# Kernel optimization log

Measured on AMD Instinct MI355X. Metric: run time of the kernel, lower is better.

## Reference

```python
import jax, jax.numpy as jnp
import numpy as np

B, T, C = 512, 256, 384
HEAD = 64

def setup_inputs() -> dict:
    key = jax.random.key(0)
    k1, k2, k3, k4 = jax.random.split(key, 4)
    x = jax.random.normal(k1, (B, T, C), dtype=jnp.float32)
    Wq = jax.random.normal(k2, (C, HEAD), dtype=jnp.float32) * (C ** -0.5)
    Wk = jax.random.normal(k3, (C, HEAD), dtype=jnp.float32) * (C ** -0.5)
    Wv = jax.random.normal(k4, (C, HEAD), dtype=jnp.float32) * (C ** -0.5)
    return {"x": x, "Wq": Wq, "Wk": Wk, "Wv": Wv}

def reference(x, Wq, Wk, Wv):
    # projections (Linear with bias=False): x @ W
    q = jnp.einsum('btc,ch->bth', x, Wq)   # [B,T,H]
    k = jnp.einsum('btc,ch->bth', x, Wk)   # [B,T,H]
    v = jnp.einsum('btc,ch->bth', x, Wv)   # [B,T,H]
    Cdim = x.shape[-1]
    # NOTE: original scales by C**-0.5 where C = nEmbd (not headSize)
    scores = jnp.einsum('bth,bsh->bts', q, k) * (Cdim ** -0.5)  # [B,T,T]
    Tlen = x.shape[1]
    causal = jnp.tril(jnp.ones((Tlen, Tlen), dtype=bool))
    scores = jnp.where(causal, scores, -jnp.inf)
    wei = jax.nn.softmax(scores, axis=-1)
    # dropout omitted (eval mode / deterministic reference)
    out = jnp.einsum('bts,bsh->bth', wei, v)  # [B,T,H]
    return out
```

## Files before the change

### kernel.cpp

```cpp
#include <hip/hip_runtime.h>

#define B_ 512
#define T_ 256
#define C_ 384
#define H_ 64
#define WT2_HALF  36864
#define WT2_TOTAL (2 * WT2_HALF)

typedef __bf16 bf16;
typedef bf16  bf16x8 __attribute__((ext_vector_type(8)));
typedef float f32x4  __attribute__((ext_vector_type(4)));

__global__ void prep_wt2(const float* __restrict__ Wq,
                         const float* __restrict__ Wk,
                         const float* __restrict__ Wv,
                         bf16* __restrict__ wt2)
{
    int idx = blockIdx.x * 256 + threadIdx.x;
    if (idx >= WT2_TOTAL) return;
    int half = idx / WT2_HALF;
    int rem  = idx % WT2_HALF;
    int s    = rem >> 3;
    int e    = rem & 7;
    int mc   = s / 24;
    int kkc  = (s % 24) ^ (mc & 7);
    int mat  = mc >> 6;
    int col  = mc & 63;
    int k    = half * 192 + kkc * 8 + e;
    const float* W = (mat == 0) ? Wq : (mat == 1) ? Wk : Wv;
    wt2[idx] = (bf16)W[k * H_ + col];
}

__device__ __forceinline__ bf16x8 cvt8(float4 a, float4 b)
{
    bf16x8 r;
    r[0] = (bf16)a.x; r[1] = (bf16)a.y; r[2] = (bf16)a.z; r[3] = (bf16)a.w;
    r[4] = (bf16)b.x; r[5] = (bf16)b.y; r[6] = (bf16)b.z; r[7] = (bf16)b.w;
    return r;
}

__device__ __forceinline__ void gload_lds16(const bf16* g, bf16* l)
{
    __builtin_amdgcn_global_load_lds(
        (const __attribute__((address_space(1))) void*)g,
        (__attribute__((address_space(3))) void*)l,
        16, 0, 0);
}

#define SWZ(row, col) ((col) ^ (((row) & 7) << 3))

__device__ __forceinline__ const bf16x8* wts_frag(const bf16* wt_s, int mc, int kk)
{
    int byte = ((mc * 192 + kk) * 2) ^ ((mc & 7) << 4);
    return reinterpret_cast<const bf16x8*>(reinterpret_cast<const char*>(wt_s) + byte);
}

template<int USE_WT>
__global__
__attribute__((amdgpu_flat_work_group_size(512, 512)))
__attribute__((amdgpu_waves_per_eu(2, 2)))
void head_fused7(const float* __restrict__ x,
                 const float* __restrict__ Wq,
                 const float* __restrict__ Wk,
                 const float* __restrict__ Wv,
                 const bf16* __restrict__ wt2,
                 float* __restrict__ out)
{
    __shared__ bf16 wt_s[3 * 64 * 192];
    __shared__ bf16 k_s[T_ * 64];
    __shared__ bf16 vT_s[H_ * 256];
    __shared__ bf16 p_s[8 * 16 * 64];

    const int tid  = threadIdx.x;
    const int wave = tid >> 6;
    const int lane = tid & 63;
    const int lr   = lane & 15;
    const int lg   = lane >> 4;

    const int b = blockIdx.x;
    const float* xb = x + (size_t)b * T_ * C_;
    bf16* pw = &p_s[wave * 16 * 64];

    const int mt0 = wave;
    const int mt1 = 15 - wave;

    bf16x8 qf[2][2];

    f32x4 acc[2][3][4];
    #pragma unroll
    for (int t = 0; t < 2; ++t)
        #pragma unroll
        for (int a = 0; a < 3; ++a)
            #pragma unroll
            for (int nw = 0; nw < 4; ++nw)
                acc[t][a][nw] = (f32x4){0.f, 0.f, 0.f, 0.f};

    #pragma unroll 1
    for (int half = 0; half < 2; ++half) {
        __syncthreads();
        if (USE_WT) {
            #pragma unroll
            for (int c = 0; c < 9; ++c) {
                const bf16* g = wt2 + half * WT2_HALF + (c * 512 + tid) * 8;
                bf16* l = wt_s + (c * 512 + wave * 64) * 8;
                gload_lds16(g, l);
            }
        } else {
            #pragma unroll
            for (int c = 0; c < 9; ++c) {
                int f16 = c * 512 + tid;
                int mc  = f16 / 24;
                int kkc = f16 % 24;
                int mat = mc >> 6, col = mc & 63;
                const float* W = (mat == 0) ? Wq : (mat == 1) ? Wk : Wv;
                bf16x8 vv;
                #pragma unroll
                for (int j = 0; j < 8; ++j)
                    vv[j] = (bf16)W[(half * 192 + kkc * 8 + j) * H_ + col];
                int byte = ((mc * 192 + kkc * 8) * 2) ^ ((mc & 7) << 4);
                *reinterpret_cast<bf16x8*>(reinterpret_cast<char*>(wt_s) + byte) = vv;
            }
        }

        bf16x8 af0[6], af1[6];
        {
            const float* xr = xb + (mt0 * 16 + lr) * C_ + half * 192 + lg * 8;
            float4 t0[6], t1[6];
            #pragma unroll
            for (int ks = 0; ks < 6; ++ks) {
                t0[ks] = *reinterpret_cast<const float4*>(xr + ks * 32);
                t1[ks] = *reinterpret_cast<const float4*>(xr + ks * 32 + 4);
            }
            #pragma unroll
            for (int ks = 0; ks < 6; ++ks) af0[ks] = cvt8(t0[ks], t1[ks]);
        }
        {
            const float* xr = xb + (mt1 * 16 + lr) * C_ + half * 192 + lg * 8;
            float4 t0[6], t1[6];
            #pragma unroll
            for (int ks = 0; ks < 6; ++ks) {
                t0[ks] = *reinterpret_cast<const float4*>(xr + ks * 32);
                t1[ks] = *reinterpret_cast<const float4*>(xr + ks * 32 + 4);
            }
            #pragma unroll
            for (int ks = 0; ks < 6; ++ks) af1[ks] = cvt8(t0[ks], t1[ks]);
        }
        __syncthreads();

        #pragma unroll
        for (int ks = 0; ks < 6; ++ks) {
            const int kk = ks * 32 + lg * 8;
            #pragma unroll
            for (int mat = 0; mat < 3; ++mat) {
                #pragma unroll
                for (int nw = 0; nw < 4; ++nw) {
                    bf16x8 bfr = *wts_frag(wt_s, mat * 64 + nw * 16 + lr, kk);
                    acc[0][mat][nw] = __builtin_amdgcn_mfma_f32_16x16x32_bf16(
                        af0[ks], bfr, acc[0][mat][nw], 0, 0, 0);
                    acc[1][mat][nw] = __builtin_amdgcn_mfma_f32_16x16x32_bf16(
                        af1[ks], bfr, acc[1][mat][nw], 0, 0, 0);
                }
            }
        }
    }

    #pragma unroll
    for (int tile = 0; tile < 2; ++tile) {
        const int mt = tile ? mt1 : mt0;
        #pragma unroll
        for (int nw = 0; nw < 4; ++nw) {
            #pragma unroll
            for (int r = 0; r < 4; ++r) {
                int row = mt * 16 + lg * 4 + r;
                int col = nw * 16 + lr;
                k_s[row * 64 + SWZ(row, col)]   = (bf16)acc[tile][1][nw][r];
                vT_s[col * 256 + SWZ(col, row)] = (bf16)acc[tile][2][nw][r];
            }
        }
        #pragma unroll
        for (int nw = 0; nw < 4; ++nw) {
            #pragma unroll
            for (int r = 0; r < 4; ++r) {
                int row = lg * 4 + r;
                pw[row * 64 + SWZ(row, nw * 16 + lr)] = (bf16)acc[tile][0][nw][r];
            }
        }
        asm volatile("s_waitcnt lgkmcnt(0)" ::: "memory");
        __builtin_amdgcn_sched_barrier(0);
        qf[tile][0] = *reinterpret_cast<const bf16x8*>(&pw[lr * 64 + SWZ(lr, lg * 8)]);
        qf[tile][1] = *reinterpret_cast<const bf16x8*>(&pw[lr * 64 + SWZ(lr, 32 + lg * 8)]);
    }
    __syncthreads();

    const float scale = 0.051031036307982884f;

    #pragma unroll
    for (int p = 0; p < 2; ++p) {
        const int mt  = p ? mt1 : mt0;
        const int nkt = mt + 1;

        float m[4], l[4];
        f32x4 oacc[4];
        #pragma unroll
        for (int r = 0; r < 4; ++r) { m[r] = -1e30f; l[r] = 0.f; }
        #pragma unroll
        for (int n = 0; n < 4; ++n) oacc[n] = (f32x4){0.f, 0.f, 0.f, 0.f};

        #pragma unroll
        for (int h = 0; h < 2; ++h) {
            const int vh = (nkt - h * 8) < 8 ? (nkt - h * 8) : 8;
            if (vh > 0) {
                float s[8][4];
                #pragma unroll
                for (int j = 0; j < 8; ++j) {
                    const int kt = h * 8 + j;
                    if (j < vh) {
                        bf16x8 kf0 = *reinterpret_cast<const bf16x8*>(
                            &k_s[(kt * 16 + lr) * 64 + SWZ(lr, lg * 8)]);
                        bf16x8 kf1 = *reinterpret_cast<const bf16x8*>(
                            &k_s[(kt * 16 + lr) * 64 + SWZ(lr, 32 + lg * 8)]);
                        f32x4 sc = (f32x4){0.f, 0.f, 0.f, 0.f};
                        sc = __builtin_amdgcn_mfma_f32_16x16x32_bf16(qf[p][0], kf0, sc, 0, 0, 0);
                        sc = __builtin_amdgcn_mfma_f32_16x16x32_bf16(qf[p][1], kf1, sc, 0, 0, 0);
                        #pragma unroll
                        for (int r = 0; r < 4; ++r) {
                            float v = sc[r] * scale;
                            if (kt == mt && lr > lg * 4 + r) v = -1e30f;
                            s[j][r] = v;
                        }
                    } else {
                        #pragma unroll
                        for (int r = 0; r < 4; ++r) s[j][r] = -1e30f;
                    }
                }

                float f[4];
                #pragma unroll
                for (int r = 0; r < 4; ++r) {
                    float pm = s[0][r];
                    #pragma unroll
                    for (int j = 1; j < 8; ++j) pm = fmaxf(pm, s[j][r]);
                    pm = fmaxf(pm, __shfl_xor(pm, 1));
                    pm = fmaxf(pm, __shfl_xor(pm, 2));
                    pm = fmaxf(pm, __shfl_xor(pm, 4));
                    pm = fmaxf(pm, __shfl_xor(pm, 8));
                    float nm = fmaxf(m[r], pm);
                    f[r] = __expf(m[r] - nm);
                    m[r] = nm;
                    l[r] *= f[r];
                }
                #pragma unroll
                for (int n = 0; n < 4; ++n)
                    #pragma unroll
                    for (int r = 0; r < 4; ++r)
                        oacc[n][r] *= f[r];

                #pragma unroll
                for (int r = 0; r < 4; ++r) {
                    float t = 0.f;
                    #pragma unroll
                    for (int j = 0; j < 8; ++j) {
                        float e = __expf(s[j][r] - m[r]);
                        s[j][r] = e;
                        t += e;
                    }
                    t += __shfl_xor(t, 1);
                    t += __shfl_xor(t, 2);
                    t += __shfl_xor(t, 4);
                    t += __shfl_xor(t, 8);
                    l[r] += t;
                }

                const int nkk = (vh + 1) >> 1;
                #pragma unroll
                for (int kkl = 0; kkl < 4; ++kkl) {
                    if (kkl < nkk) {
                        const int kk = h * 4 + kkl;
                        #pragma unroll
                        for (int r = 0; r < 4; ++r) {
                            int row = lg * 4 + r;
                            pw[row * 64 + SWZ(row, lr)]      = (bf16)s[2 * kkl][r];
                            pw[row * 64 + SWZ(row, 16 + lr)] = (bf16)s[2 * kkl + 1][r];
                        }
                        asm volatile("s_waitcnt lgkmcnt(0)" ::: "memory");
                        __builtin_amdgcn_sched_barrier(0);
                        bf16x8 pf = *reinterpret_cast<const bf16x8*>(
                            &pw[lr * 64 + SWZ(lr, lg * 8)]);
                        #pragma unroll
                        for (int n = 0; n < 4; ++n) {
                            bf16x8 vf = *reinterpret_cast<const bf16x8*>(
                                &vT_s[(n * 16 + lr) * 256 + SWZ(lr, kk * 32 + lg * 8)]);
                            oacc[n] = __builtin_amdgcn_mfma_f32_16x16x32_bf16(pf, vf, oacc[n], 0, 0, 0);
                        }
                    }
                }
            }
        }

        float rin[4];
        #pragma unroll
        for (int r = 0; r < 4; ++r) rin[r] = 1.0f / l[r];
        float* op = out + ((size_t)b * T_ + mt * 16) * H_;
        #pragma unroll
        for (int n = 0; n < 4; ++n)
            #pragma unroll
            for (int r = 0; r < 4; ++r)
                op[(lg * 4 + r) * H_ + n * 16 + lr] = oacc[n][r] * rin[r];
    }
}

extern "C" void kernel_launch(void* const* d_in, const int* in_sizes, int n_in,
                              void* d_out, int out_size, void* d_ws, size_t ws_size,
                              hipStream_t stream)
{
    (void)in_sizes; (void)n_in; (void)out_size;
    const float* x  = (const float*)d_in[0];
    const float* Wq = (const float*)d_in[1];
    const float* Wk = (const float*)d_in[2];
    const float* Wv = (const float*)d_in[3];
    float* o = (float*)d_out;

    if (ws_size >= (size_t)(WT2_TOTAL * sizeof(bf16))) {
        bf16* wt2 = (bf16*)d_ws;
        prep_wt2<<<dim3((WT2_TOTAL + 255) / 256), dim3(256), 0, stream>>>(Wq, Wk, Wv, wt2);
        head_fused7<1><<<dim3(B_), dim3(512), 0, stream>>>(x, Wq, Wk, Wv, wt2, o);
    } else {
        head_fused7<0><<<dim3(B_), dim3(512), 0, stream>>>(x, Wq, Wk, Wv, nullptr, o);
    }
}
```

Measured before the change: 78.12 us.

## Split fused attention into projection and attention kernels via bf16 workspace

```diff
diff --git a/kernel.cpp b/kernel.cpp
--- a/kernel.cpp
+++ b/kernel.cpp
@@ -4,12 +4,19 @@
 #define T_ 256
 #define C_ 384
 #define H_ 64
+
+typedef __bf16 bf16;
+typedef bf16  bf16x8 __attribute__((ext_vector_type(8)));
+typedef bf16  bf16x4 __attribute__((ext_vector_type(4)));
+typedef float f32x4  __attribute__((ext_vector_type(4)));
+
 #define WT2_HALF  36864
 #define WT2_TOTAL (2 * WT2_HALF)
-
-typedef __bf16 bf16;
-typedef bf16  bf16x8 __attribute__((ext_vector_type(8)));
-typedef float f32x4  __attribute__((ext_vector_type(4)));
+#define QKV_ELEMS (B_ * T_ * H_)
+#define Q_OFF  (1u << 20)
+#define K_OFF  (Q_OFF + (unsigned)QKV_ELEMS * 2u)
+#define V_OFF  (K_OFF + (unsigned)QKV_ELEMS * 2u)
+#define WS_NEED ((size_t)V_OFF + (size_t)QKV_ELEMS * 2u)
 
 __global__ void prep_wt2(const float* __restrict__ Wq,
                          const float* __restrict__ Wk,
@@ -56,20 +63,17 @@
 }
 
 template<int USE_WT>
-__global__
-__attribute__((amdgpu_flat_work_group_size(512, 512)))
-__attribute__((amdgpu_waves_per_eu(2, 2)))
-void head_fused7(const float* __restrict__ x,
+__global__ __launch_bounds__(512, 2)
+void proj_kernel(const float* __restrict__ x,
                  const float* __restrict__ Wq,
                  const float* __restrict__ Wk,
                  const float* __restrict__ Wv,
                  const bf16* __restrict__ wt2,
-                 float* __restrict__ out)
+                 bf16* __restrict__ q_ws,
+                 bf16* __restrict__ k_ws,
+                 bf16* __restrict__ vT_ws)
 {
     __shared__ bf16 wt_s[3 * 64 * 192];
-    __shared__ bf16 k_s[T_ * 64];
-    __shared__ bf16 vT_s[H_ * 256];
-    __shared__ bf16 p_s[8 * 16 * 64];
 
     const int tid  = threadIdx.x;
     const int wave = tid >> 6;
@@ -79,12 +83,7 @@
 
     const int b = blockIdx.x;
     const float* xb = x + (size_t)b * T_ * C_;
-    bf16* pw = &p_s[wave * 16 * 64];
-
-    const int mt0 = wave;
-    const int mt1 = 15 - wave;
-
-    bf16x8 qf[2][2];
+    const int mt0 = wave, mt1 = 15 - wave;
 
     f32x4 acc[2][3][4];
     #pragma unroll
@@ -97,7 +96,7 @@
 
     #pragma unroll 1
     for (int half = 0; half < 2; ++half) {
-        __syncthreads();
+        if (half) __syncthreads();
         if (USE_WT) {
             #pragma unroll
             for (int c = 0; c < 9; ++c) {
@@ -121,34 +120,18 @@
                 *reinterpret_cast<bf16x8*>(reinterpret_cast<char*>(wt_s) + byte) = vv;
             }
         }
-
-        bf16x8 af0[6], af1[6];
-        {
-            const float* xr = xb + (mt0 * 16 + lr) * C_ + half * 192 + lg * 8;
-            float4 t0[6], t1[6];
-            #pragma unroll
-            for (int ks = 0; ks < 6; ++ks) {
-                t0[ks] = *reinterpret_cast<const float4*>(xr + ks * 32);
-                t1[ks] = *reinterpret_cast<const float4*>(xr + ks * 32 + 4);
-            }
-            #pragma unroll
-            for (int ks = 0; ks < 6; ++ks) af0[ks] = cvt8(t0[ks], t1[ks]);
-        }
-        {
-            const float* xr = xb + (mt1 * 16 + lr) * C_ + half * 192 + lg * 8;
-            float4 t0[6], t1[6];
-            #pragma unroll
-            for (int ks = 0; ks < 6; ++ks) {
-                t0[ks] = *reinterpret_cast<const float4*>(xr + ks * 32);
-                t1[ks] = *reinterpret_cast<const float4*>(xr + ks * 32 + 4);
-            }
-            #pragma unroll
-            for (int ks = 0; ks < 6; ++ks) af1[ks] = cvt8(t0[ks], t1[ks]);
-        }
         __syncthreads();
 
+        const float* xr0 = xb + (mt0 * 16 + lr) * C_ + half * 192 + lg * 8;
+        const float* xr1 = xb + (mt1 * 16 + lr) * C_ + half * 192 + lg * 8;
         #pragma unroll
         for (int ks = 0; ks < 6; ++ks) {
+            float4 a0 = *reinterpret_cast<const float4*>(xr0 + ks * 32);
+            float4 a1 = *reinterpret_cast<const float4*>(xr0 + ks * 32 + 4);
+            float4 b0 = *reinterpret_cast<const float4*>(xr1 + ks * 32);
+            float4 b1 = *reinterpret_cast<const float4*>(xr1 + ks * 32 + 4);
+            bf16x8 af0 = cvt8(a0, a1);
+            bf16x8 af1 = cvt8(b0, b1);
             const int kk = ks * 32 + lg * 8;
             #pragma unroll
             for (int mat = 0; mat < 3; ++mat) {
@@ -156,14 +139,17 @@
                 for (int nw = 0; nw < 4; ++nw) {
                     bf16x8 bfr = *wts_frag(wt_s, mat * 64 + nw * 16 + lr, kk);
                     acc[0][mat][nw] = __builtin_amdgcn_mfma_f32_16x16x32_bf16(
-                        af0[ks], bfr, acc[0][mat][nw], 0, 0, 0);
+                        af0, bfr, acc[0][mat][nw], 0, 0, 0);
                     acc[1][mat][nw] = __builtin_amdgcn_mfma_f32_16x16x32_bf16(
-                        af1[ks], bfr, acc[1][mat][nw], 0, 0, 0);
+                        af1, bfr, acc[1][mat][nw], 0, 0, 0);
                 }
             }
         }
     }
 
+    bf16* qb = q_ws  + (size_t)b * T_ * H_;
+    bf16* kb = k_ws  + (size_t)b * T_ * H_;
+    bf16* vb = vT_ws + (size_t)b * T_ * H_;
     #pragma unroll
     for (int tile = 0; tile < 2; ++tile) {
         const int mt = tile ? mt1 : mt0;
@@ -173,31 +159,47 @@
             for (int r = 0; r < 4; ++r) {
                 int row = mt * 16 + lg * 4 + r;
                 int col = nw * 16 + lr;
-                k_s[row * 64 + SWZ(row, col)]   = (bf16)acc[tile][1][nw][r];
-                vT_s[col * 256 + SWZ(col, row)] = (bf16)acc[tile][2][nw][r];
-            }
+                qb[row * H_ + col] = (bf16)acc[tile][0][nw][r];
+                kb[row * H_ + col] = (bf16)acc[tile][1][nw][r];
+            }
+            bf16x4 pv;
+            #pragma unroll
+            for (int r = 0; r < 4; ++r) pv[r] = (bf16)acc[tile][2][nw][r];
+            *reinterpret_cast<bf16x4*>(vb + (nw * 16 + lr) * T_ + mt * 16 + lg * 4) = pv;
         }
-        #pragma unroll
-        for (int nw = 0; nw < 4; ++nw) {
-            #pragma unroll
-            for (int r = 0; r < 4; ++r) {
-                int row = lg * 4 + r;
-                pw[row * 64 + SWZ(row, nw * 16 + lr)] = (bf16)acc[tile][0][nw][r];
-            }
-        }
-        asm volatile("s_waitcnt lgkmcnt(0)" ::: "memory");
-        __builtin_amdgcn_sched_barrier(0);
-        qf[tile][0] = *reinterpret_cast<const bf16x8*>(&pw[lr * 64 + SWZ(lr, lg * 8)]);
-        qf[tile][1] = *reinterpret_cast<const bf16x8*>(&pw[lr * 64 + SWZ(lr, 32 + lg * 8)]);
     }
-    __syncthreads();
+}
+
+__global__ __launch_bounds__(256, 4)
+void attn_kernel(const bf16* __restrict__ q_ws,
+                 const bf16* __restrict__ k_ws,
+                 const bf16* __restrict__ vT_ws,
+                 float* __restrict__ out)
+{
+    __shared__ bf16 p_s[4 * 16 * 64];
+
+    const int tid  = threadIdx.x;
+    const int wave = tid >> 6;
+    const int lane = tid & 63;
+    const int lr   = lane & 15;
+    const int lg   = lane >> 4;
+
+    const int b = blockIdx.x;
+    const bf16* qb = q_ws  + (size_t)b * T_ * H_;
+    const bf16* kb = k_ws  + (size_t)b * T_ * H_;
+    const bf16* vb = vT_ws + (size_t)b * T_ * H_;
+    bf16* pw = &p_s[wave * 16 * 64];
 
     const float scale = 0.051031036307982884f;
 
-    #pragma unroll
-    for (int p = 0; p < 2; ++p) {
-        const int mt  = p ? mt1 : mt0;
+    #pragma unroll 1
+    for (int p = 0; p < 4; ++p) {
+        const int mt  = (p == 0) ? wave : (p == 1) ? 7 - wave
+                      : (p == 2) ? 8 + wave : 15 - wave;
         const int nkt = mt + 1;
+
+        bf16x8 qf0 = *reinterpret_cast<const bf16x8*>(qb + (mt * 16 + lr) * H_ + lg * 8);
+        bf16x8 qf1 = *reinterpret_cast<const bf16x8*>(qb + (mt * 16 + lr) * H_ + 32 + lg * 8);
 
         float m[4], l[4];
         f32x4 oacc[4];
@@ -216,12 +218,12 @@
                     const int kt = h * 8 + j;
                     if (j < vh) {
                         bf16x8 kf0 = *reinterpret_cast<const bf16x8*>(
-                            &k_s[(kt * 16 + lr) * 64 + SWZ(lr, lg * 8)]);
+                            kb + (kt * 16 + lr) * H_ + lg * 8);
                         bf16x8 kf1 = *reinterpret_cast<const bf16x8*>(
-                            &k_s[(kt * 16 + lr) * 64 + SWZ(lr, 32 + lg * 8)]);
+                            kb + (kt * 16 + lr) * H_ + 32 + lg * 8);
                         f32x4 sc = (f32x4){0.f, 0.f, 0.f, 0.f};
-                        sc = __builtin_amdgcn_mfma_f32_16x16x32_bf16(qf[p][0], kf0, sc, 0, 0, 0);
-                        sc = __builtin_amdgcn_mfma_f32_16x16x32_bf16(qf[p][1], kf1, sc, 0, 0, 0);
+                        sc = __builtin_amdgcn_mfma_f32_16x16x32_bf16(qf0, kf0, sc, 0, 0, 0);
+                        sc = __builtin_amdgcn_mfma_f32_16x16x32_bf16(qf1, kf1, sc, 0, 0, 0);
                         #pragma unroll
                         for (int r = 0; r < 4; ++r) {
                             float v = sc[r] * scale;
@@ -289,7 +291,7 @@
                         #pragma unroll
                         for (int n = 0; n < 4; ++n) {
                             bf16x8 vf = *reinterpret_cast<const bf16x8*>(
-                                &vT_s[(n * 16 + lr) * 256 + SWZ(lr, kk * 32 + lg * 8)]);
+                                vb + (n * 16 + lr) * T_ + kk * 32 + lg * 8);
                             oacc[n] = __builtin_amdgcn_mfma_f32_16x16x32_bf16(pf, vf, oacc[n], 0, 0, 0);
                         }
                     }
@@ -320,11 +322,19 @@
     const float* Wv = (const float*)d_in[3];
     float* o = (float*)d_out;
 
-    if (ws_size >= (size_t)(WT2_TOTAL * sizeof(bf16))) {
-        bf16* wt2 = (bf16*)d_ws;
+    if (ws_size >= WS_NEED) {
+        bf16* wt2  = (bf16*)d_ws;
+        bf16* q_ws = (bf16*)((char*)d_ws + Q_OFF);
+        bf16* k_ws = (bf16*)((char*)d_ws + K_OFF);
+        bf16* v_ws = (bf16*)((char*)d_ws + V_OFF);
         prep_wt2<<<dim3((WT2_TOTAL + 255) / 256), dim3(256), 0, stream>>>(Wq, Wk, Wv, wt2);
-        head_fused7<1><<<dim3(B_), dim3(512), 0, stream>>>(x, Wq, Wk, Wv, wt2, o);
+        proj_kernel<1><<<dim3(B_), dim3(512), 0, stream>>>(x, Wq, Wk, Wv, wt2, q_ws, k_ws, v_ws);
+        attn_kernel<<<dim3(B_), dim3(256), 0, stream>>>(q_ws, k_ws, v_ws, o);
     } else {
-        head_fused7<0><<<dim3(B_), dim3(512), 0, stream>>>(x, Wq, Wk, Wv, nullptr, o);
+        bf16* q_ws = (bf16*)d_ws;
+        bf16* k_ws = q_ws + QKV_ELEMS;
+        bf16* v_ws = k_ws + QKV_ELEMS;
+        proj_kernel<0><<<dim3(B_), dim3(512), 0, stream>>>(x, Wq, Wk, Wv, nullptr, q_ws, k_ws, v_ws);
+        attn_kernel<<<dim3(B_), dim3(256), 0, stream>>>(q_ws, k_ws, v_ws, o);
     }
 }
```

Result: slower. 144.3 us (+84.7%).

## Split weight staging into three K-chunks and alias LDS to fit two blocks per CU

Applied to the files above, without the earlier changes.

```diff
diff --git a/kernel.cpp b/kernel.cpp
--- a/kernel.cpp
+++ b/kernel.cpp
@@ -4,31 +4,34 @@
 #define T_ 256
 #define C_ 384
 #define H_ 64
-#define WT2_HALF  36864
-#define WT2_TOTAL (2 * WT2_HALF)
 
 typedef __bf16 bf16;
 typedef bf16  bf16x8 __attribute__((ext_vector_type(8)));
 typedef float f32x4  __attribute__((ext_vector_type(4)));
 
-__global__ void prep_wt2(const float* __restrict__ Wq,
+#define NCHUNK     3
+#define CHUNK_K    128
+#define WT3_CHUNK  24576
+#define WT3_TOTAL  (NCHUNK * WT3_CHUNK)
+
+__global__ void prep_wt3(const float* __restrict__ Wq,
                          const float* __restrict__ Wk,
                          const float* __restrict__ Wv,
-                         bf16* __restrict__ wt2)
+                         bf16* __restrict__ wt3)
 {
     int idx = blockIdx.x * 256 + threadIdx.x;
-    if (idx >= WT2_TOTAL) return;
-    int half = idx / WT2_HALF;
-    int rem  = idx % WT2_HALF;
-    int s    = rem >> 3;
-    int e    = rem & 7;
-    int mc   = s / 24;
-    int kkc  = (s % 24) ^ (mc & 7);
-    int mat  = mc >> 6;
-    int col  = mc & 63;
-    int k    = half * 192 + kkc * 8 + e;
+    if (idx >= WT3_TOTAL) return;
+    int chunk = idx / WT3_CHUNK;
+    int rem   = idx % WT3_CHUNK;
+    int s     = rem >> 3;
+    int e     = rem & 7;
+    int mc    = s >> 4;
+    int kkc   = (s & 15) ^ (mc & 7);
+    int mat   = mc >> 6;
+    int col   = mc & 63;
+    int k     = chunk * CHUNK_K + kkc * 8 + e;
     const float* W = (mat == 0) ? Wq : (mat == 1) ? Wk : Wv;
-    wt2[idx] = (bf16)W[k * H_ + col];
+    wt3[idx] = (bf16)W[k * H_ + col];
 }
 
 __device__ __forceinline__ bf16x8 cvt8(float4 a, float4 b)
@@ -51,25 +54,25 @@
 
 __device__ __forceinline__ const bf16x8* wts_frag(const bf16* wt_s, int mc, int kk)
 {
-    int byte = ((mc * 192 + kk) * 2) ^ ((mc & 7) << 4);
+    int byte = ((mc * CHUNK_K + kk) * 2) ^ ((mc & 7) << 4);
     return reinterpret_cast<const bf16x8*>(reinterpret_cast<const char*>(wt_s) + byte);
 }
 
 template<int USE_WT>
-__global__
-__attribute__((amdgpu_flat_work_group_size(512, 512)))
-__attribute__((amdgpu_waves_per_eu(2, 2)))
-void head_fused7(const float* __restrict__ x,
-                 const float* __restrict__ Wq,
-                 const float* __restrict__ Wk,
-                 const float* __restrict__ Wv,
-                 const bf16* __restrict__ wt2,
-                 float* __restrict__ out)
-{
-    __shared__ bf16 wt_s[3 * 64 * 192];
-    __shared__ bf16 k_s[T_ * 64];
-    __shared__ bf16 vT_s[H_ * 256];
+__global__ __launch_bounds__(512, 2)
+void head_fused11(const float* __restrict__ x,
+                  const float* __restrict__ Wq,
+                  const float* __restrict__ Wk,
+                  const float* __restrict__ Wv,
+                  const bf16* __restrict__ wt3,
+                  float* __restrict__ out)
+{
+    __shared__ bf16 lds_u[32768];
     __shared__ bf16 p_s[8 * 16 * 64];
+
+    bf16* wt_s = lds_u;
+    bf16* k_s  = lds_u;
+    bf16* vT_s = lds_u + 16384;
 
     const int tid  = threadIdx.x;
     const int wave = tid >> 6;
@@ -81,9 +84,7 @@
     const float* xb = x + (size_t)b * T_ * C_;
     bf16* pw = &p_s[wave * 16 * 64];
 
-    const int mt0 = wave;
-    const int mt1 = 15 - wave;
-
+    const int mt0 = wave, mt1 = 15 - wave;
     bf16x8 qf[2][2];
 
     f32x4 acc[2][3][4];
@@ -96,59 +97,43 @@
                 acc[t][a][nw] = (f32x4){0.f, 0.f, 0.f, 0.f};
 
     #pragma unroll 1
-    for (int half = 0; half < 2; ++half) {
-        __syncthreads();
+    for (int chunk = 0; chunk < NCHUNK; ++chunk) {
+        if (chunk) __syncthreads();
         if (USE_WT) {
             #pragma unroll
-            for (int c = 0; c < 9; ++c) {
-                const bf16* g = wt2 + half * WT2_HALF + (c * 512 + tid) * 8;
+            for (int c = 0; c < 6; ++c) {
+                const bf16* g = wt3 + chunk * WT3_CHUNK + (c * 512 + tid) * 8;
                 bf16* l = wt_s + (c * 512 + wave * 64) * 8;
                 gload_lds16(g, l);
             }
         } else {
             #pragma unroll
-            for (int c = 0; c < 9; ++c) {
+            for (int c = 0; c < 6; ++c) {
                 int f16 = c * 512 + tid;
-                int mc  = f16 / 24;
-                int kkc = f16 % 24;
+                int mc  = f16 >> 4;
+                int kkc = f16 & 15;
                 int mat = mc >> 6, col = mc & 63;
                 const float* W = (mat == 0) ? Wq : (mat == 1) ? Wk : Wv;
                 bf16x8 vv;
                 #pragma unroll
                 for (int j = 0; j < 8; ++j)
-                    vv[j] = (bf16)W[(half * 192 + kkc * 8 + j) * H_ + col];
-                int byte = ((mc * 192 + kkc * 8) * 2) ^ ((mc & 7) << 4);
+                    vv[j] = (bf16)W[(chunk * CHUNK_K + kkc * 8 + j) * H_ + col];
+                int byte = ((mc * CHUNK_K + kkc * 8) * 2) ^ ((mc & 7) << 4);
                 *reinterpret_cast<bf16x8*>(reinterpret_cast<char*>(wt_s) + byte) = vv;
             }
         }
-
-        bf16x8 af0[6], af1[6];
-        {
-            const float* xr = xb + (mt0 * 16 + lr) * C_ + half * 192 + lg * 8;
-            float4 t0[6], t1[6];
-            #pragma unroll
-            for (int ks = 0; ks < 6; ++ks) {
-                t0[ks] = *reinterpret_cast<const float4*>(xr + ks * 32);
-                t1[ks] = *reinterpret_cast<const float4*>(xr + ks * 32 + 4);
-            }
-            #pragma unroll
-            for (int ks = 0; ks < 6; ++ks) af0[ks] = cvt8(t0[ks], t1[ks]);
-        }
-        {
-            const float* xr = xb + (mt1 * 16 + lr) * C_ + half * 192 + lg * 8;
-            float4 t0[6], t1[6];
-            #pragma unroll
-            for (int ks = 0; ks < 6; ++ks) {
-                t0[ks] = *reinterpret_cast<const float4*>(xr + ks * 32);
-                t1[ks] = *reinterpret_cast<const float4*>(xr + ks * 32 + 4);
-            }
-            #pragma unroll
-            for (int ks = 0; ks < 6; ++ks) af1[ks] = cvt8(t0[ks], t1[ks]);
-        }
         __syncthreads();
 
-        #pragma unroll
-        for (int ks = 0; ks < 6; ++ks) {
+        const float* xr0 = xb + (mt0 * 16 + lr) * C_ + chunk * CHUNK_K + lg * 8;
+        const float* xr1 = xb + (mt1 * 16 + lr) * C_ + chunk * CHUNK_K + lg * 8;
+        #pragma unroll
+        for (int ks = 0; ks < 4; ++ks) {
+            float4 a0 = *reinterpret_cast<const float4*>(xr0 + ks * 32);
+            float4 a1 = *reinterpret_cast<const float4*>(xr0 + ks * 32 + 4);
+            float4 b0 = *reinterpret_cast<const float4*>(xr1 + ks * 32);
+            float4 b1 = *reinterpret_cast<const float4*>(xr1 + ks * 32 + 4);
+            bf16x8 af0 = cvt8(a0, a1);
+            bf16x8 af1 = cvt8(b0, b1);
             const int kk = ks * 32 + lg * 8;
             #pragma unroll
             for (int mat = 0; mat < 3; ++mat) {
@@ -156,13 +141,14 @@
                 for (int nw = 0; nw < 4; ++nw) {
                     bf16x8 bfr = *wts_frag(wt_s, mat * 64 + nw * 16 + lr, kk);
                     acc[0][mat][nw] = __builtin_amdgcn_mfma_f32_16x16x32_bf16(
-                        af0[ks], bfr, acc[0][mat][nw], 0, 0, 0);
+                        af0, bfr, acc[0][mat][nw], 0, 0, 0);
                     acc[1][mat][nw] = __builtin_amdgcn_mfma_f32_16x16x32_bf16(
-                        af1[ks], bfr, acc[1][mat][nw], 0, 0, 0);
+                        af1, bfr, acc[1][mat][nw], 0, 0, 0);
                 }
             }
         }
     }
+    __syncthreads();
 
     #pragma unroll
     for (int tile = 0; tile < 2; ++tile) {
@@ -189,6 +175,8 @@
         __builtin_amdgcn_sched_barrier(0);
         qf[tile][0] = *reinterpret_cast<const bf16x8*>(&pw[lr * 64 + SWZ(lr, lg * 8)]);
         qf[tile][1] = *reinterpret_cast<const bf16x8*>(&pw[lr * 64 + SWZ(lr, 32 + lg * 8)]);
+        asm volatile("s_waitcnt lgkmcnt(0)" ::: "memory");
+        __builtin_amdgcn_sched_barrier(0);
     }
     __syncthreads();
 
@@ -320,11 +308,11 @@
     const float* Wv = (const float*)d_in[3];
     float* o = (float*)d_out;
 
-    if (ws_size >= (size_t)(WT2_TOTAL * sizeof(bf16))) {
-        bf16* wt2 = (bf16*)d_ws;
-        prep_wt2<<<dim3((WT2_TOTAL + 255) / 256), dim3(256), 0, stream>>>(Wq, Wk, Wv, wt2);
-        head_fused7<1><<<dim3(B_), dim3(512), 0, stream>>>(x, Wq, Wk, Wv, wt2, o);
+    if (ws_size >= (size_t)(WT3_TOTAL * sizeof(bf16))) {
+        bf16* wt3 = (bf16*)d_ws;
+        prep_wt3<<<dim3((WT3_TOTAL + 255) / 256), dim3(256), 0, stream>>>(Wq, Wk, Wv, wt3);
+        head_fused11<1><<<dim3(B_), dim3(512), 0, stream>>>(x, Wq, Wk, Wv, wt3, o);
     } else {
-        head_fused7<0><<<dim3(B_), dim3(512), 0, stream>>>(x, Wq, Wk, Wv, nullptr, o);
+        head_fused11<0><<<dim3(B_), dim3(512), 0, stream>>>(x, Wq, Wk, Wv, nullptr, o);
     }
 }
```

Result: faster. 66.85 us (-14.4%).
